# Performance work log

Measured on AMD Instinct MI355X. Metric: run time of the kernel, lower is better.

## Reference

```python
import jax, jax.numpy as jnp
import numpy as np

EPS = 1e-5

def setup_inputs() -> dict:
    key = jax.random.key(0)
    ks = jax.random.split(key, 6)
    N, M, F, K = 100000, 12, 128, 64
    atom_in_fea = jax.random.normal(ks[0], (N, F), dtype=jnp.float32)
    nbr_fea = jax.random.normal(ks[1], (N, M, K), dtype=jnp.float32)
    nbr_fea_idx = jax.random.randint(ks[2], (N, M), 0, N, dtype=jnp.int64)
    # Linear(2F+K -> 2F): torch stores weight [out, in]
    W = jax.random.normal(ks[3], (2 * F, 2 * F + K), dtype=jnp.float32) * 0.02
    b = jax.random.normal(ks[4], (2 * F,), dtype=jnp.float32) * 0.02
    bn1_gamma = jnp.ones((2 * F,), dtype=jnp.float32)
    bn1_beta = jnp.zeros((2 * F,), dtype=jnp.float32)
    bn2_gamma = jnp.ones((F,), dtype=jnp.float32)
    bn2_beta = jnp.zeros((F,), dtype=jnp.float32)
    return {"atom_in_fea": atom_in_fea, "nbr_fea": nbr_fea, "nbr_fea_idx": nbr_fea_idx,
            "W": W, "b": b, "bn1_gamma": bn1_gamma, "bn1_beta": bn1_beta,
            "bn2_gamma": bn2_gamma, "bn2_beta": bn2_beta}

def _batchnorm(x, gamma, beta):
    # training-mode BatchNorm1d: biased batch variance, eps=1e-5
    mean = jnp.mean(x, axis=0)
    var = jnp.var(x, axis=0)
    return (x - mean) * jax.lax.rsqrt(var + EPS) * gamma + beta

def reference(atom_in_fea, nbr_fea, nbr_fea_idx, W, b, bn1_gamma, bn1_beta, bn2_gamma, bn2_beta):
    N, M = nbr_fea_idx.shape
    F = atom_in_fea.shape[1]
    atom_nbr_fea = atom_in_fea[nbr_fea_idx]                      # [N, M, F] gather
    atom_self = jnp.broadcast_to(atom_in_fea[:, None, :], (N, M, F))
    total = jnp.concatenate([atom_self, atom_nbr_fea, nbr_fea], axis=2)  # [N, M, 2F+K]
    gated = jnp.einsum('nmk,ok->nmo', total, W) + b              # [N, M, 2F]
    gated = _batchnorm(gated.reshape(-1, 2 * F), bn1_gamma, bn1_beta).reshape(N, M, 2 * F)
    nbr_filter, nbr_core = jnp.split(gated, 2, axis=2)
    nbr_sumed = jnp.sum(jax.nn.sigmoid(nbr_filter) * jax.nn.relu(nbr_core), axis=1)  # [N, F]
    nbr_sumed = _batchnorm(nbr_sumed, bn2_gamma, bn2_beta)
    return jax.nn.relu(atom_in_fea + nbr_sumed)
```

## Files before the change

kernel.cpp:

```cpp
#include <hip/hip_runtime.h>

typedef __bf16 bf16x8 __attribute__((ext_vector_type(8)));
typedef __bf16 bf16x4 __attribute__((ext_vector_type(4)));
typedef float  f32x4  __attribute__((ext_vector_type(4)));

#define CIN   320
#define APAD  328
#define ROWS  96
#define SPAD  264

__global__ void detect_kernel(const unsigned short* __restrict__ atom_h,
                              const unsigned* __restrict__ idx_w, int* __restrict__ flags)
{
    const int lane = threadIdx.x;
    int f32 = 0;
    for (int i = lane; i < 256; i += 64) {
        const int e = (atom_h[i] >> 7) & 0xFF;
        if (e >= 134) f32 = 1;
    }
    const unsigned long long m32 = __ballot(f32);
    const int hi = (idx_w[2 * lane + 1] != 0) ? 1 : 0;
    const unsigned long long mhi = __ballot(hi);
    if (lane == 0) { flags[0] = m32 ? 1 : 0; flags[1] = mhi ? 0 : 1; }
}

__global__ __launch_bounds__(256) void convert_bf16(const void* __restrict__ src,
    __bf16* __restrict__ dst, long n8, const int* __restrict__ flags)
{
    const long t = (long)blockIdx.x * 256 + threadIdx.x;
    if (t >= n8) return;
    const long i = t * 8;
    if (flags[0]) {
        const float* s = (const float*)src;
        bf16x8 o;
#pragma unroll
        for (int j = 0; j < 8; ++j) o[j] = (__bf16)s[i + j];
        *(bf16x8*)&dst[i] = o;
    } else {
        *(uint4*)&dst[i] = *(const uint4*)((const char*)src + i * 2);
    }
}

template<int MODE>
__global__ __launch_bounds__(256, 2) void gemm_conv(
    const __bf16* __restrict__ atomb, const void* __restrict__ nbrp,
    const void* __restrict__ idxp, const __bf16* __restrict__ Wb,
    const int* __restrict__ flags,
    float* __restrict__ stats1, const float* __restrict__ coef1,
    __bf16* __restrict__ gws, float* __restrict__ nsum)
{
    __shared__ __align__(16) char smem[ROWS * APAD * 2];
    __bf16* Alds = (__bf16*)smem;

    const int tid = threadIdx.x;
    const int blk = blockIdx.x;
    const long rowbase = (long)blk * ROWS;
    const int  n0 = blk * 8;
    const int  isf32 = flags[0];
    const int  isi64 = flags[1];

    {
        const int c  = tid & 15;
        const int rs = tid >> 4;
#pragma unroll
        for (int it = 0; it < 6; ++it) {
            const int lr = rs + it * 16;
            const int nn = n0 + lr / 12;
            *(uint4*)&Alds[lr * APAD + c * 8] =
                *(const uint4*)&atomb[(long)nn * 128 + c * 8];
            const long r = rowbase + lr;
            const int j = isi64 ? (int)((const long long*)idxp)[r]
                                : ((const int*)idxp)[r];
            *(uint4*)&Alds[lr * APAD + 128 + c * 8] =
                *(const uint4*)&atomb[(long)j * 128 + c * 8];
        }
        if (isf32) {
            const float* nf = (const float*)nbrp;
#pragma unroll
            for (int it = 0; it < 6; ++it) {
                const int lr = rs + it * 16;
                f32x4 v = *(const f32x4*)&nf[(rowbase + lr) * 64 + c * 4];
                bf16x4 o;
#pragma unroll
                for (int j = 0; j < 4; ++j) o[j] = (__bf16)v[j];
                *(bf16x4*)&Alds[lr * APAD + 256 + c * 4] = o;
            }
        } else {
            const __bf16* nb = (const __bf16*)nbrp;
            const int c2  = tid & 7;
            const int rs2 = tid >> 3;
#pragma unroll
            for (int it = 0; it < 3; ++it) {
                const int lr = rs2 + it * 32;
                *(uint4*)&Alds[lr * APAD + 256 + c2 * 8] =
                    *(const uint4*)&nb[(rowbase + lr) * 64 + c2 * 8];
            }
        }
    }
    __syncthreads();

    const int lane = tid & 63;
    const int wv   = tid >> 6;
    const int quad = lane >> 4;
    const int lrow = lane & 15;
    const int cb0  = wv * 32;

    int cols[4];
    const __bf16* wp[4];
#pragma unroll
    for (int ct = 0; ct < 4; ++ct) {
        cols[ct] = cb0 + ((ct & 1) ? 16 : 0) + ((ct & 2) ? 128 : 0) + lrow;
        wp[ct] = Wb + (long)cols[ct] * CIN + quad * 8;
    }

    f32x4 acc[6][4] = {};
    bf16x8 bcur[4], bnxt[4];
#pragma unroll
    for (int ct = 0; ct < 4; ++ct) bcur[ct] = *(const bf16x8*)(wp[ct]);

#pragma unroll
    for (int kk = 0; kk < 10; ++kk) {
        const int k0 = kk * 32;
        if (kk < 9) {
#pragma unroll
            for (int ct = 0; ct < 4; ++ct)
                bnxt[ct] = *(const bf16x8*)(wp[ct] + k0 + 32);
        }
#pragma unroll
        for (int rt = 0; rt < 6; ++rt) {
            bf16x8 afrag = *(const bf16x8*)&Alds[(rt * 16 + lrow) * APAD + k0 + quad * 8];
#pragma unroll
            for (int ct = 0; ct < 4; ++ct)
                acc[rt][ct] = __builtin_amdgcn_mfma_f32_16x16x32_bf16(
                                  afrag, bcur[ct], acc[rt][ct], 0, 0, 0);
        }
        if (kk < 9) {
#pragma unroll
            for (int ct = 0; ct < 4; ++ct) bcur[ct] = bnxt[ct];
        }
    }

    if (MODE <= 1) {
        float* st = stats1 + (blk & 63) * 512;
#pragma unroll
        for (int ct = 0; ct < 4; ++ct) {
            float s = 0.f, ss = 0.f;
#pragma unroll
            for (int rt = 0; rt < 6; ++rt)
#pragma unroll
                for (int r = 0; r < 4; ++r) {
                    const float v = acc[rt][ct][r];
                    s += v; ss += v * v;
                }
            s += __shfl_xor(s, 16); ss += __shfl_xor(ss, 16);
            s += __shfl_xor(s, 32); ss += __shfl_xor(ss, 32);
            if (quad == 0) {
                atomicAdd(&st[cols[ct]], s);
                atomicAdd(&st[256 + cols[ct]], ss);
            }
        }
        if (MODE == 1) {
            __syncthreads();
            __bf16* S = (__bf16*)smem;
#pragma unroll
            for (int rt = 0; rt < 6; ++rt)
#pragma unroll
                for (int ct = 0; ct < 4; ++ct)
#pragma unroll
                    for (int r = 0; r < 4; ++r)
                        S[(rt * 16 + quad * 4 + r) * SPAD + cols[ct]] = (__bf16)acc[rt][ct][r];
            __syncthreads();
            const __bf16* Sr = (const __bf16*)smem;
            __bf16* dst = gws + rowbase * 256;
#pragma unroll
            for (int it = 0; it < 12; ++it) {
                const int e = tid * 8 + it * 2048;
                *(bf16x8*)&dst[e] = *(const bf16x8*)&Sr[(e >> 8) * SPAD + (e & 255)];
            }
        }
    } else {
        __syncthreads();
        float* sumbuf = (float*)smem;
#pragma unroll
        for (int e = tid; e < 1024; e += 256) sumbuf[e] = 0.f;
        __syncthreads();
#pragma unroll
        for (int p = 0; p < 2; ++p) {
            const int cF = cb0 + p * 16 + lrow;
            const float aF = coef1[cF],       bF = coef1[256 + cF];
            const float aC = coef1[128 + cF], bC = coef1[384 + cF];
#pragma unroll
            for (int rt = 0; rt < 6; ++rt)
#pragma unroll
                for (int r = 0; r < 4; ++r) {
                    const float gF = aF * acc[rt][p][r] + bF;
                    const float gC = aC * acc[rt][p + 2][r] + bC;
                    const float val = (1.f / (1.f + __expf(-gF))) * fmaxf(gC, 0.f);
                    const int lr = rt * 16 + quad * 4 + r;
                    atomicAdd(&sumbuf[(lr / 12) * 128 + cF], val);
                }
        }
        __syncthreads();
#pragma unroll
        for (int e = tid; e < 1024; e += 256)
            nsum[(long)(n0 + (e >> 7)) * 128 + (e & 127)] = sumbuf[e];
    }
}

__global__ void reduce_bn1(const float* __restrict__ stats1, const void* __restrict__ gamma,
                           const void* __restrict__ beta, float* __restrict__ coef1,
                           const int* __restrict__ flags)
{
    const int c = threadIdx.x;
    const int isf32 = flags[0];
    float s = 0.f, ss = 0.f;
    for (int b = 0; b < 64; ++b) { s += stats1[b * 512 + c]; ss += stats1[b * 512 + 256 + c]; }
    const float inv  = 1.f / 1200000.f;
    const float mean = s * inv;
    const float var  = ss * inv - mean * mean;
    const float g  = isf32 ? ((const float*)gamma)[c] : (float)((const __bf16*)gamma)[c];
    const float bb = isf32 ? ((const float*)beta)[c]  : (float)((const __bf16*)beta)[c];
    const float A = g * rsqrtf(var + 1e-5f);
    coef1[c]       = A;
    coef1[256 + c] = bb - A * mean;
}

__global__ __launch_bounds__(256) void apply_gated(const __bf16* __restrict__ g,
    const float* __restrict__ coef1, float* __restrict__ nsum)
{
    const int tid  = threadIdx.x;
    const int nloc = tid >> 4;
    const int fc   = (tid & 15) * 8;
    const long n   = (long)blockIdx.x * 16 + nloc;
    float aF[8], bF[8], aC[8], bC[8];
#pragma unroll
    for (int j = 0; j < 8; ++j) {
        aF[j] = coef1[fc + j];       bF[j] = coef1[256 + fc + j];
        aC[j] = coef1[128 + fc + j]; bC[j] = coef1[384 + fc + j];
    }
    float s[8] = {};
    const __bf16* base = g + n * (12 * 256);
#pragma unroll
    for (int m = 0; m < 12; ++m) {
        bf16x8 vF = *(const bf16x8*)&base[m * 256 + fc];
        bf16x8 vC = *(const bf16x8*)&base[m * 256 + 128 + fc];
#pragma unroll
        for (int j = 0; j < 8; ++j) {
            const float gF = aF[j] * (float)vF[j] + bF[j];
            const float gC = aC[j] * (float)vC[j] + bC[j];
            s[j] += (1.f / (1.f + __expf(-gF))) * fmaxf(gC, 0.f);
        }
    }
    f32x4 s0 = {s[0], s[1], s[2], s[3]}, s1 = {s[4], s[5], s[6], s[7]};
    *(f32x4*)&nsum[n * 128 + fc]     = s0;
    *(f32x4*)&nsum[n * 128 + fc + 4] = s1;
}

__global__ __launch_bounds__(256) void bn2_stats(const float* __restrict__ nsum,
                                                 float* __restrict__ stats2)
{
    __shared__ float ls[256], lss[256];
    const int tid = threadIdx.x;
    float s = 0.f, ss = 0.f;
    const long stride = (long)gridDim.x * 256;
    for (long i = (long)blockIdx.x * 256 + tid; i < 12800000L; i += stride) {
        const float v = nsum[i]; s += v; ss += v * v;
    }
    ls[tid] = s; lss[tid] = ss;
    __syncthreads();
    if (tid < 128) {
        atomicAdd(&stats2[tid],       ls[tid] + ls[tid + 128]);
        atomicAdd(&stats2[128 + tid], lss[tid] + lss[tid + 128]);
    }
}

__global__ void reduce_bn2(const float* __restrict__ stats2, const void* __restrict__ gamma,
                           const void* __restrict__ beta, float* __restrict__ coef2,
                           const int* __restrict__ flags)
{
    const int c = threadIdx.x;
    const int isf32 = flags[0];
    const float inv  = 1.f / 100000.f;
    const float mean = stats2[c] * inv;
    const float var  = stats2[128 + c] * inv - mean * mean;
    const float g  = isf32 ? ((const float*)gamma)[c] : (float)((const __bf16*)gamma)[c];
    const float bb = isf32 ? ((const float*)beta)[c]  : (float)((const __bf16*)beta)[c];
    const float A = g * rsqrtf(var + 1e-5f);
    coef2[c]       = A;
    coef2[128 + c] = bb - A * mean;
}

__global__ __launch_bounds__(256) void final_out(const __bf16* __restrict__ atomb,
    const float* __restrict__ nsum, const float* __restrict__ coef2,
    void* __restrict__ outp, const int* __restrict__ flags)
{
    const long i = ((long)blockIdx.x * 256 + threadIdx.x) * 8;
    const int f0 = (int)(i & 127);
    bf16x8 a  = *(const bf16x8*)&atomb[i];
    f32x4  u0 = *(const f32x4*)&nsum[i];
    f32x4  u1 = *(const f32x4*)&nsum[i + 4];
    float v[8];
#pragma unroll
    for (int j = 0; j < 8; ++j) {
        const float A  = coef2[f0 + j];
        const float B  = coef2[128 + f0 + j];
        const float ns = (j < 4) ? u0[j] : u1[j - 4];
        v[j] = fmaxf((float)a[j] + A * ns + B, 0.f);
    }
    if (flags[0]) {
        float* o = (float*)outp;
        f32x4 w0 = {v[0], v[1], v[2], v[3]}, w1 = {v[4], v[5], v[6], v[7]};
        *(f32x4*)&o[i]     = w0;
        *(f32x4*)&o[i + 4] = w1;
    } else {
        __bf16* o = (__bf16*)outp;
        bf16x8 w;
#pragma unroll
        for (int j = 0; j < 8; ++j) w[j] = (__bf16)v[j];
        *(bf16x8*)&o[i] = w;
    }
}

extern "C" void kernel_launch(void* const* d_in, const int* in_sizes, int n_in,
                              void* d_out, int out_size, void* d_ws, size_t ws_size,
                              hipStream_t stream)
{
    const void* atom = d_in[0];
    const void* nbr  = d_in[1];
    const void* idxp = d_in[2];
    const void* W    = d_in[3];
    const void* g1   = d_in[5];
    const void* b1   = d_in[6];
    const void* g2   = d_in[7];
    const void* b2   = d_in[8];

    char* ws = (char*)d_ws;
    int*    flags  = (int*)ws;
    float*  stats1 = (float*)(ws + 1024);
    float*  coef1  = (float*)(ws + 132096);
    float*  stats2 = (float*)(ws + 134144);
    float*  coef2  = (float*)(ws + 135168);
    __bf16* atomb  = (__bf16*)(ws + 136192);
    __bf16* Wb     = (__bf16*)(ws + 25736192);
    float*  nsum   = (float*)(ws + 25900032);
    __bf16* gws    = (__bf16*)(ws + 77100032);

    const size_t need_big = 77100032UL + 614400000UL;

    hipMemsetAsync(ws, 0, 136192, stream);
    detect_kernel<<<1, 64, 0, stream>>>((const unsigned short*)atom, (const unsigned*)idxp, flags);
    convert_bf16<<<6250, 256, 0, stream>>>(atom, atomb, 1600000L, flags);
    convert_bf16<<<40, 256, 0, stream>>>(W, Wb, 10240L, flags);

    if (ws_size >= need_big) {
        gemm_conv<1><<<12500, 256, 0, stream>>>(atomb, nbr, idxp, Wb, flags,
                                                stats1, nullptr, gws, nullptr);
        reduce_bn1<<<1, 256, 0, stream>>>(stats1, g1, b1, coef1, flags);
        apply_gated<<<6250, 256, 0, stream>>>(gws, coef1, nsum);
    } else {
        gemm_conv<0><<<12500, 256, 0, stream>>>(atomb, nbr, idxp, Wb, flags,
                                                stats1, nullptr, nullptr, nullptr);
        reduce_bn1<<<1, 256, 0, stream>>>(stats1, g1, b1, coef1, flags);
        gemm_conv<2><<<12500, 256, 0, stream>>>(atomb, nbr, idxp, Wb, flags,
                                                nullptr, coef1, nullptr, nsum);
    }
    bn2_stats<<<512, 256, 0, stream>>>(nsum, stats2);
    reduce_bn2<<<1, 128, 0, stream>>>(stats2, g2, b2, coef2, flags);
    final_out<<<6250, 256, 0, stream>>>(atomb, nsum, coef2, d_out, flags);
}
```

Before: 1.061 ms.

## Load GEMM A-tiles via global_load_lds with swizzled LDS and dedup self rows

The fused gather-GEMM kernel now loads gathered neighbour rows and edge features straight into LDS with global_load_lds, using an XOR swizzle. It stores the 8 self-atom rows once instead of replicating them 12 times. Blocks grow to 512 threads (8 waves), each wave computing a 16-column filter/core pair. The intermediate gated tensor is written in MFMA fragment order, and apply_gated is rewritten to consume that layout with LDS atomic reductions. The aim is less LDS footprint, fewer register round-trips on the load path, and higher occupancy, at the cost of LDS atomics in the epilogue and a layout coupling between the two kernels.

```diff
diff --git a/kernel.cpp b/kernel.cpp
--- a/kernel.cpp
+++ b/kernel.cpp
@@ -4,10 +4,16 @@
 typedef __bf16 bf16x4 __attribute__((ext_vector_type(4)));
 typedef float  f32x4  __attribute__((ext_vector_type(4)));
 
-#define CIN   320
-#define APAD  328
-#define ROWS  96
-#define SPAD  264
+#define CIN 320
+#define GATHER_OFF 0
+#define EDGE_OFF   24576
+#define SELF_OFF   36864
+#define SMEM_BYTES 38912
+
+#define GLOAD_LDS16(gsrc, ldst)                                              \
+    __builtin_amdgcn_global_load_lds(                                        \
+        (__attribute__((address_space(1))) void*)(void*)(gsrc),              \
+        (__attribute__((address_space(3))) void*)(ldst), 16, 0, 0)
 
 __global__ void detect_kernel(const unsigned short* __restrict__ atom_h,
                               const unsigned* __restrict__ idx_w, int* __restrict__ flags)
@@ -42,168 +48,173 @@
 }
 
 template<int MODE>
-__global__ __launch_bounds__(256, 2) void gemm_conv(
+__global__ __launch_bounds__(512, 4) void gemm_conv(
     const __bf16* __restrict__ atomb, const void* __restrict__ nbrp,
     const void* __restrict__ idxp, const __bf16* __restrict__ Wb,
     const int* __restrict__ flags,
     float* __restrict__ stats1, const float* __restrict__ coef1,
     __bf16* __restrict__ gws, float* __restrict__ nsum)
 {
-    __shared__ __align__(16) char smem[ROWS * APAD * 2];
-    __bf16* Alds = (__bf16*)smem;
+    __shared__ __align__(16) char smem[SMEM_BYTES];
 
     const int tid = threadIdx.x;
     const int blk = blockIdx.x;
-    const long rowbase = (long)blk * ROWS;
+    const long rowbase = (long)blk * 96;
     const int  n0 = blk * 8;
     const int  isf32 = flags[0];
     const int  isi64 = flags[1];
-
-    {
-        const int c  = tid & 15;
-        const int rs = tid >> 4;
-#pragma unroll
-        for (int it = 0; it < 6; ++it) {
-            const int lr = rs + it * 16;
-            const int nn = n0 + lr / 12;
-            *(uint4*)&Alds[lr * APAD + c * 8] =
-                *(const uint4*)&atomb[(long)nn * 128 + c * 8];
-            const long r = rowbase + lr;
-            const int j = isi64 ? (int)((const long long*)idxp)[r]
-                                : ((const int*)idxp)[r];
-            *(uint4*)&Alds[lr * APAD + 128 + c * 8] =
-                *(const uint4*)&atomb[(long)j * 128 + c * 8];
-        }
-        if (isf32) {
-            const float* nf = (const float*)nbrp;
-#pragma unroll
-            for (int it = 0; it < 6; ++it) {
-                const int lr = rs + it * 16;
-                f32x4 v = *(const f32x4*)&nf[(rowbase + lr) * 64 + c * 4];
-                bf16x4 o;
-#pragma unroll
-                for (int j = 0; j < 4; ++j) o[j] = (__bf16)v[j];
-                *(bf16x4*)&Alds[lr * APAD + 256 + c * 4] = o;
-            }
-        } else {
-            const __bf16* nb = (const __bf16*)nbrp;
-            const int c2  = tid & 7;
-            const int rs2 = tid >> 3;
-#pragma unroll
-            for (int it = 0; it < 3; ++it) {
-                const int lr = rs2 + it * 32;
-                *(uint4*)&Alds[lr * APAD + 256 + c2 * 8] =
-                    *(const uint4*)&nb[(rowbase + lr) * 64 + c2 * 8];
-            }
-        }
-    }
-    __syncthreads();
 
     const int lane = tid & 63;
     const int wv   = tid >> 6;
     const int quad = lane >> 4;
     const int lrow = lane & 15;
-    const int cb0  = wv * 32;
-
-    int cols[4];
-    const __bf16* wp[4];
-#pragma unroll
-    for (int ct = 0; ct < 4; ++ct) {
-        cols[ct] = cb0 + ((ct & 1) ? 16 : 0) + ((ct & 2) ? 128 : 0) + lrow;
-        wp[ct] = Wb + (long)cols[ct] * CIN + quad * 8;
-    }
-
-    f32x4 acc[6][4] = {};
-    bf16x8 bcur[4], bnxt[4];
-#pragma unroll
-    for (int ct = 0; ct < 4; ++ct) bcur[ct] = *(const bf16x8*)(wp[ct]);
+
+    if (wv < 2) {
+        const int row = wv * 4 + (lane >> 4);
+        GLOAD_LDS16(atomb + (long)(n0 + row) * 128 + (lane & 15) * 8,
+                    smem + SELF_OFF + wv * 1024);
+    }
+    long jrow[3]; int grow[3];
+#pragma unroll
+    for (int i = 0; i < 3; ++i) {
+        const int t = wv + i * 8;
+        grow[i] = 4 * t + (lane >> 4);
+        jrow[i] = isi64 ? (long)((const long long*)idxp)[rowbase + grow[i]]
+                        : (long)((const int*)idxp)[rowbase + grow[i]];
+    }
+#pragma unroll
+    for (int i = 0; i < 3; ++i) {
+        const int t = wv + i * 8;
+        const int chunk = ((lane & 15) << 4) ^ ((grow[i] & 7) << 4);
+        GLOAD_LDS16(atomb + jrow[i] * 128 + (chunk >> 1),
+                    smem + GATHER_OFF + t * 1024);
+    }
+    if (isf32) {
+        const float* nf = (const float*)nbrp;
+#pragma unroll
+        for (int rnd = 0; rnd < 2; ++rnd) {
+            const int task = tid + rnd * 512;
+            if (task < 768) {
+                const int c = task & 7, row = task >> 3;
+                const float* sp = &nf[(rowbase + row) * 64 + c * 8];
+                f32x4 v0 = *(const f32x4*)sp;
+                f32x4 v1 = *(const f32x4*)(sp + 4);
+                bf16x8 o;
+#pragma unroll
+                for (int j = 0; j < 4; ++j) { o[j] = (__bf16)v0[j]; o[j + 4] = (__bf16)v1[j]; }
+                *(bf16x8*)(smem + EDGE_OFF + row * 128 + ((c ^ (row & 7)) << 4)) = o;
+            }
+        }
+    } else {
+        const __bf16* nb = (const __bf16*)nbrp;
+#pragma unroll
+        for (int i = 0; i < 2; ++i) {
+            const int t = wv + i * 8;
+            if (t < 12) {
+                const int row = 8 * t + (lane >> 3);
+                const int c = lane & 7;
+                const int chunk = (c << 4) ^ ((row & 7) << 4);
+                GLOAD_LDS16(nb + (rowbase + row) * 64 + (chunk >> 1),
+                            smem + EDGE_OFF + t * 1024);
+            }
+        }
+    }
+    __syncthreads();
+
+    const int cF = wv * 16 + lrow;
+    const __bf16* wpF = Wb + (long)cF * CIN + quad * 8;
+    const __bf16* wpC = Wb + (long)(128 + cF) * CIN + quad * 8;
+
+    int arow[6], aatom[6];
+#pragma unroll
+    for (int rt = 0; rt < 6; ++rt) {
+        arow[rt]  = rt * 16 + lrow;
+        aatom[rt] = (arow[rt] * 171) >> 11;
+    }
+
+    f32x4 acc[6][2] = {};
+    bf16x8 bF = *(const bf16x8*)wpF;
+    bf16x8 bC = *(const bf16x8*)wpC;
+    bf16x8 bFn, bCn;
 
 #pragma unroll
     for (int kk = 0; kk < 10; ++kk) {
-        const int k0 = kk * 32;
         if (kk < 9) {
-#pragma unroll
-            for (int ct = 0; ct < 4; ++ct)
-                bnxt[ct] = *(const bf16x8*)(wp[ct] + k0 + 32);
+            bFn = *(const bf16x8*)(wpF + (kk + 1) * 32);
+            bCn = *(const bf16x8*)(wpC + (kk + 1) * 32);
         }
 #pragma unroll
         for (int rt = 0; rt < 6; ++rt) {
-            bf16x8 afrag = *(const bf16x8*)&Alds[(rt * 16 + lrow) * APAD + k0 + quad * 8];
-#pragma unroll
-            for (int ct = 0; ct < 4; ++ct)
-                acc[rt][ct] = __builtin_amdgcn_mfma_f32_16x16x32_bf16(
-                                  afrag, bcur[ct], acc[rt][ct], 0, 0, 0);
-        }
-        if (kk < 9) {
-#pragma unroll
-            for (int ct = 0; ct < 4; ++ct) bcur[ct] = bnxt[ct];
-        }
+            int addr;
+            if (kk < 4)
+                addr = SELF_OFF + aatom[rt] * 256 + kk * 64 + quad * 16;
+            else if (kk < 8)
+                addr = GATHER_OFF + arow[rt] * 256 + ((((kk - 4) * 4 + quad) ^ (arow[rt] & 7)) << 4);
+            else
+                addr = EDGE_OFF + arow[rt] * 128 + ((((kk - 8) * 4 + quad) ^ (arow[rt] & 7)) << 4);
+            const bf16x8 afrag = *(const bf16x8*)(smem + addr);
+            acc[rt][0] = __builtin_amdgcn_mfma_f32_16x16x32_bf16(afrag, bF, acc[rt][0], 0, 0, 0);
+            acc[rt][1] = __builtin_amdgcn_mfma_f32_16x16x32_bf16(afrag, bC, acc[rt][1], 0, 0, 0);
+        }
+        if (kk < 9) { bF = bFn; bC = bCn; }
     }
 
     if (MODE <= 1) {
         float* st = stats1 + (blk & 63) * 512;
 #pragma unroll
-        for (int ct = 0; ct < 4; ++ct) {
+        for (int p = 0; p < 2; ++p) {
             float s = 0.f, ss = 0.f;
 #pragma unroll
             for (int rt = 0; rt < 6; ++rt)
 #pragma unroll
                 for (int r = 0; r < 4; ++r) {
-                    const float v = acc[rt][ct][r];
+                    const float v = acc[rt][p][r];
                     s += v; ss += v * v;
                 }
             s += __shfl_xor(s, 16); ss += __shfl_xor(ss, 16);
             s += __shfl_xor(s, 32); ss += __shfl_xor(ss, 32);
             if (quad == 0) {
-                atomicAdd(&st[cols[ct]], s);
-                atomicAdd(&st[256 + cols[ct]], ss);
+                atomicAdd(&st[p * 128 + cF], s);
+                atomicAdd(&st[256 + p * 128 + cF], ss);
             }
         }
         if (MODE == 1) {
-            __syncthreads();
-            __bf16* S = (__bf16*)smem;
-#pragma unroll
-            for (int rt = 0; rt < 6; ++rt)
-#pragma unroll
-                for (int ct = 0; ct < 4; ++ct)
-#pragma unroll
-                    for (int r = 0; r < 4; ++r)
-                        S[(rt * 16 + quad * 4 + r) * SPAD + cols[ct]] = (__bf16)acc[rt][ct][r];
-            __syncthreads();
-            const __bf16* Sr = (const __bf16*)smem;
-            __bf16* dst = gws + rowbase * 256;
-#pragma unroll
-            for (int it = 0; it < 12; ++it) {
-                const int e = tid * 8 + it * 2048;
-                *(bf16x8*)&dst[e] = *(const bf16x8*)&Sr[(e >> 8) * SPAD + (e & 255)];
+            char* dst = (char*)gws + (long)blk * 49152;
+#pragma unroll
+            for (int rt = 0; rt < 6; ++rt) {
+                unsigned u[4];
+#pragma unroll
+                for (int r = 0; r < 4; ++r) {
+                    const unsigned short fb =
+                        __builtin_bit_cast(unsigned short, (__bf16)acc[rt][0][r]);
+                    const unsigned short cb =
+                        __builtin_bit_cast(unsigned short, (__bf16)acc[rt][1][r]);
+                    u[r] = (unsigned)fb | ((unsigned)cb << 16);
+                }
+                *(uint4*)(dst + rt * 8192 + tid * 16) = *(const uint4*)u;
             }
         }
     } else {
         __syncthreads();
         float* sumbuf = (float*)smem;
-#pragma unroll
-        for (int e = tid; e < 1024; e += 256) sumbuf[e] = 0.f;
+        sumbuf[tid] = 0.f; sumbuf[tid + 512] = 0.f;
         __syncthreads();
-#pragma unroll
-        for (int p = 0; p < 2; ++p) {
-            const int cF = cb0 + p * 16 + lrow;
-            const float aF = coef1[cF],       bF = coef1[256 + cF];
-            const float aC = coef1[128 + cF], bC = coef1[384 + cF];
-#pragma unroll
-            for (int rt = 0; rt < 6; ++rt)
-#pragma unroll
-                for (int r = 0; r < 4; ++r) {
-                    const float gF = aF * acc[rt][p][r] + bF;
-                    const float gC = aC * acc[rt][p + 2][r] + bC;
-                    const float val = (1.f / (1.f + __expf(-gF))) * fmaxf(gC, 0.f);
-                    const int lr = rt * 16 + quad * 4 + r;
-                    atomicAdd(&sumbuf[(lr / 12) * 128 + cF], val);
-                }
-        }
+        const float aF = coef1[cF],       bFc = coef1[256 + cF];
+        const float aC = coef1[128 + cF], bCc = coef1[384 + cF];
+#pragma unroll
+        for (int rt = 0; rt < 6; ++rt)
+#pragma unroll
+            for (int r = 0; r < 4; ++r) {
+                const int row  = rt * 16 + quad * 4 + r;
+                const int atom = (row * 171) >> 11;
+                const float gF = aF * acc[rt][0][r] + bFc;
+                const float gC = aC * acc[rt][1][r] + bCc;
+                const float val = (1.f / (1.f + __expf(-gF))) * fmaxf(gC, 0.f);
+                atomicAdd(&sumbuf[atom * 128 + cF], val);
+            }
         __syncthreads();
-#pragma unroll
-        for (int e = tid; e < 1024; e += 256)
-            nsum[(long)(n0 + (e >> 7)) * 128 + (e & 127)] = sumbuf[e];
+        nsum[(long)n0 * 128 + tid]       = sumbuf[tid];
+        nsum[(long)n0 * 128 + 512 + tid] = sumbuf[tid + 512];
     }
 }
 
@@ -225,35 +236,40 @@
     coef1[256 + c] = bb - A * mean;
 }
 
-__global__ __launch_bounds__(256) void apply_gated(const __bf16* __restrict__ g,
+__global__ __launch_bounds__(512) void apply_gated(const __bf16* __restrict__ g,
     const float* __restrict__ coef1, float* __restrict__ nsum)
 {
+    __shared__ float sumbuf[1024];
     const int tid  = threadIdx.x;
-    const int nloc = tid >> 4;
-    const int fc   = (tid & 15) * 8;
-    const long n   = (long)blockIdx.x * 16 + nloc;
-    float aF[8], bF[8], aC[8], bC[8];
-#pragma unroll
-    for (int j = 0; j < 8; ++j) {
-        aF[j] = coef1[fc + j];       bF[j] = coef1[256 + fc + j];
-        aC[j] = coef1[128 + fc + j]; bC[j] = coef1[384 + fc + j];
-    }
-    float s[8] = {};
-    const __bf16* base = g + n * (12 * 256);
-#pragma unroll
-    for (int m = 0; m < 12; ++m) {
-        bf16x8 vF = *(const bf16x8*)&base[m * 256 + fc];
-        bf16x8 vC = *(const bf16x8*)&base[m * 256 + 128 + fc];
-#pragma unroll
-        for (int j = 0; j < 8; ++j) {
-            const float gF = aF[j] * (float)vF[j] + bF[j];
-            const float gC = aC[j] * (float)vC[j] + bC[j];
-            s[j] += (1.f / (1.f + __expf(-gF))) * fmaxf(gC, 0.f);
-        }
-    }
-    f32x4 s0 = {s[0], s[1], s[2], s[3]}, s1 = {s[4], s[5], s[6], s[7]};
-    *(f32x4*)&nsum[n * 128 + fc]     = s0;
-    *(f32x4*)&nsum[n * 128 + fc + 4] = s1;
+    const int blk  = blockIdx.x;
+    const int lane = tid & 63;
+    const int wv   = tid >> 6;
+    const int quad = lane >> 4;
+    const int lrow = lane & 15;
+    const int cF   = wv * 16 + lrow;
+    sumbuf[tid] = 0.f; sumbuf[tid + 512] = 0.f;
+    __syncthreads();
+    const float aF = coef1[cF],       bF = coef1[256 + cF];
+    const float aC = coef1[128 + cF], bC = coef1[384 + cF];
+    const char* src = (const char*)g + (long)blk * 49152;
+#pragma unroll
+    for (int rt = 0; rt < 6; ++rt) {
+        const uint4 w = *(const uint4*)(src + rt * 8192 + tid * 16);
+        const unsigned u[4] = {w.x, w.y, w.z, w.w};
+#pragma unroll
+        for (int r = 0; r < 4; ++r) {
+            const int row  = rt * 16 + quad * 4 + r;
+            const int atom = (row * 171) >> 11;
+            const float gF = aF * (float)__builtin_bit_cast(__bf16, (unsigned short)(u[r] & 0xFFFFu)) + bF;
+            const float gC = aC * (float)__builtin_bit_cast(__bf16, (unsigned short)(u[r] >> 16)) + bC;
+            const float val = (1.f / (1.f + __expf(-gF))) * fmaxf(gC, 0.f);
+            atomicAdd(&sumbuf[atom * 128 + cF], val);
+        }
+    }
+    __syncthreads();
+    const long n0 = (long)blk * 8;
+    nsum[n0 * 128 + tid]       = sumbuf[tid];
+    nsum[n0 * 128 + 512 + tid] = sumbuf[tid + 512];
 }
 
 __global__ __launch_bounds__(256) void bn2_stats(const float* __restrict__ nsum,
@@ -353,15 +369,15 @@
     convert_bf16<<<40, 256, 0, stream>>>(W, Wb, 10240L, flags);
 
     if (ws_size >= need_big) {
-        gemm_conv<1><<<12500, 256, 0, stream>>>(atomb, nbr, idxp, Wb, flags,
+        gemm_conv<1><<<12500, 512, 0, stream>>>(atomb, nbr, idxp, Wb, flags,
                                                 stats1, nullptr, gws, nullptr);
         reduce_bn1<<<1, 256, 0, stream>>>(stats1, g1, b1, coef1, flags);
-        apply_gated<<<6250, 256, 0, stream>>>(gws, coef1, nsum);
-    } else {
-        gemm_conv<0><<<12500, 256, 0, stream>>>(atomb, nbr, idxp, Wb, flags,
+        apply_gated<<<12500, 512, 0, stream>>>(gws, coef1, nsum);
+    } else {
+        gemm_conv<0><<<12500, 512, 0, stream>>>(atomb, nbr, idxp, Wb, flags,
                                                 stats1, nullptr, nullptr, nullptr);
         reduce_bn1<<<1, 256, 0, stream>>>(stats1, g1, b1, coef1, flags);
-        gemm_conv<2><<<12500, 256, 0, stream>>>(atomb, nbr, idxp, Wb, flags,
+        gemm_conv<2><<<12500, 512, 0, stream>>>(atomb, nbr, idxp, Wb, flags,
                                                 nullptr, coef1, nullptr, nsum);
     }
     bn2_stats<<<512, 256, 0, stream>>>(nsum, stats2);
```

New measurement: 1.616 ms. +52.3%, slower.
